# Optimization experiments

Hardware: AMD Instinct MI355X
Metric: run time of the kernel (lower is better)

The kernel has to match this reference:

```python
import jax, jax.numpy as jnp
import numpy as np


def _scan_dir(x, A, B, reverse):
    """First-order linear recurrence h_i = A*h_{i-1} + B*x_i along last axis (W).
    x: [Bsz, C, H, W]; A, B: [C]. reverse=True scans right-to-left but returns
    states in original index order (matching torch scan_backward)."""
    xs = jnp.moveaxis(x, -1, 0)  # [W, Bsz, C, H]
    Ab = A[None, :, None]
    Bb = B[None, :, None]
    def step(h, xi):
        h = Ab * h + Bb * xi
        return h, h
    h0 = jnp.zeros_like(xs[0])
    _, hs = jax.lax.scan(step, h0, xs, reverse=reverse)
    return jnp.moveaxis(hs, 0, -1)  # [Bsz, C, H, W]


def _conv1x1(x, W, b):
    # x: [B,Cin,H,W], W: [Cout,Cin], b: [Cout]
    return jnp.einsum('bchw,dc->bdhw', x, W) + b[None, :, None, None]


def setup_inputs() -> dict:
    key = jax.random.key(0)
    ks = jax.random.split(key, 10)
    B, C, H, W = 8, 64, 128, 128
    D = 128  # hidden_dim
    return {
        'F_in': jax.random.normal(ks[0], (B, C, H, W), dtype=jnp.float32),
        'prior': jax.random.uniform(ks[1], (B, 1, H, W), dtype=jnp.float32),
        'Wi': jax.random.normal(ks[2], (D, C), dtype=jnp.float32) * 0.05,
        'bi': jnp.zeros((D,), dtype=jnp.float32),
        'A_param': jax.random.normal(ks[3], (D,), dtype=jnp.float32),
        'B_param': jax.random.normal(ks[4], (D,), dtype=jnp.float32),
        'alpha': jnp.float32(0.1),
        'gamma': jnp.float32(0.1),
        'Wf': jax.random.normal(ks[5], (D, 4 * D), dtype=jnp.float32) * 0.05,
        'bf': jnp.zeros((D,), dtype=jnp.float32),
        'Wo': jax.random.normal(ks[6], (C, D), dtype=jnp.float32) * 0.05,
        'bo': jnp.zeros((C,), dtype=jnp.float32),
    }


def reference(F_in, prior, Wi, bi, A_param, B_param, alpha, gamma, Wf, bf, Wo, bo):
    # prior has 1 channel, repeated to C channels (prior already matches HxW)
    prior_r = jnp.broadcast_to(prior, F_in.shape)
    F_mod = F_in + alpha * prior_r
    x = _conv1x1(F_mod, Wi, bi)  # [B, D, H, W]
    A = jnp.tanh(A_param)
    Bp = B_param
    h_lr = _scan_dir(x, A, Bp, reverse=False)
    h_rl = _scan_dir(x, A, Bp, reverse=True)
    xt = jnp.swapaxes(x, 2, 3)  # scan over H axis
    h_tb = jnp.swapaxes(_scan_dir(xt, A, Bp, reverse=False), 2, 3)
    h_bt = jnp.swapaxes(_scan_dir(xt, A, Bp, reverse=True), 2, 3)
    h = jnp.concatenate([h_lr, h_rl, h_tb, h_bt], axis=1)  # [B, 4D, H, W]
    h = _conv1x1(h, Wf, bf)   # fusion -> [B, D, H, W]
    out = _conv1x1(h, Wo, bo)  # output_proj -> [B, C, H, W]
    return F_mod + gamma * out
```

## Files before the change

### kernel.cpp

```cpp
#include <hip/hip_runtime.h>
#include <hip/hip_bf16.h>

typedef unsigned int u32;
typedef unsigned short u16;
typedef float f32x2 __attribute__((ext_vector_type(2)));
typedef float f32x4 __attribute__((ext_vector_type(4)));
using bf16x8 = __attribute__((ext_vector_type(8))) short;
using f32x4v = __attribute__((ext_vector_type(4))) float;

#define DEVINL __device__ __forceinline__

constexpr int SCAN_LDS = 32768;
constexpr int XS = 132;
constexpr int LDS_X = 128 * XS * 2;

DEVINL float bf2f(u16 u) { union { u32 i; float f; } v; v.i = ((u32)u) << 16; return v.f; }
DEVINL float bf2f_lo(u32 u) { union { u32 i; float f; } v; v.i = u << 16; return v.f; }
DEVINL float bf2f_hi(u32 u) { union { u32 i; float f; } v; v.i = u & 0xffff0000u; return v.f; }
DEVINL u16 f2bf(float f) {
  __hip_bfloat16 h = __float2bfloat16(f);
  u16 r; __builtin_memcpy(&r, &h, 2); return r;
}
DEVINL u32 pack2(float a, float b) { return (u32)f2bf(a) | ((u32)f2bf(b) << 16); }

__global__ __launch_bounds__(256) void k_pre(
    const float* __restrict__ Wf, const float* __restrict__ Wo,
    const float* __restrict__ bf_, const float* __restrict__ bo,
    const float* __restrict__ A_param, const float* __restrict__ Wi,
    float* __restrict__ A_t, float* __restrict__ beff,
    u16* __restrict__ Mrow, u16* __restrict__ Wi_bf) {
  const int wg = blockIdx.x, t = threadIdx.x;
  if (wg < 128) {
    const int idx = wg * 256 + t;
    const int cout = idx >> 9;
    const int k = idx & 511;
    float s = 0.f;
    for (int d = 0; d < 128; ++d) s = fmaf(Wo[cout * 128 + d], Wf[d * 512 + k], s);
    const int dir = k >> 7, dm = k & 127;
    Mrow[(dir * 64 + cout) * 128 + dm] = f2bf(s);
  } else if (wg == 128) {
    if (t < 128) A_t[t] = tanhf(A_param[t]);
    if (t < 64) {
      float s = bo[t];
      for (int d = 0; d < 128; ++d) s = fmaf(Wo[t * 128 + d], bf_[d], s);
      beff[t] = s;
    }
  } else {
#pragma unroll
    for (int k = 0; k < 32; ++k) {
      const int i = t + k * 256;
      Wi_bf[i] = f2bf(Wi[i]);
    }
  }
}

extern __shared__ char smem[];

template <bool REV>
DEVINL void scan_col128(char* buf, int dp, float A0, float A1, float B0, float B1) {
  float h0 = 0.f, h1 = 0.f;
  const u32 cb = (u32)(dp * 4);
  u32 nx[8];
#pragma unroll
  for (int j = 0; j < 8; ++j) {
    const int i = REV ? (127 - j) : j;
    nx[j] = *(const u32*)(buf + i * 128 + (cb ^ ((u32)((i & 7) << 4))));
  }
  for (int ib = 0; ib < 128; ib += 8) {
    u32 cur[8];
#pragma unroll
    for (int j = 0; j < 8; ++j) cur[j] = nx[j];
    if (ib + 8 < 128) {
#pragma unroll
      for (int j = 0; j < 8; ++j) {
        const int i = REV ? (127 - (ib + 8 + j)) : (ib + 8 + j);
        nx[j] = *(const u32*)(buf + i * 128 + (cb ^ ((u32)((i & 7) << 4))));
      }
    }
#pragma unroll
    for (int j = 0; j < 8; ++j) {
      const int i = REV ? (127 - (ib + j)) : (ib + j);
      h0 = fmaf(A0, h0, B0 * bf2f_lo(cur[j]));
      h1 = fmaf(A1, h1, B1 * bf2f_hi(cur[j]));
      *(u32*)(buf + i * 128 + (cb ^ ((u32)((i & 7) << 4)))) = pack2(h0, h1);
    }
  }
}

DEVINL void combine64(const char* buf, const u16* __restrict__ Mrow, int dir, int e,
                      int lane, int wv, f32x4v (&acc2)[4][2]) {
  const int l15 = lane & 15, kg = lane >> 4;
#pragma unroll
  for (int ks = 0; ks < 2; ++ks) {
    bf16x8 afr[4], bfr[2];
#pragma unroll
    for (int ct = 0; ct < 4; ++ct)
      afr[ct] = *(const bf16x8*)(Mrow + ((size_t)dir * 64 + ct * 16 + l15) * 128 + e * 64 + ks * 32 + kg * 8);
#pragma unroll
    for (int pt = 0; pt < 2; ++pt) {
      const int row = wv * 32 + pt * 16 + l15;
      bfr[pt] = *(const bf16x8*)(buf + row * 128 + ((u32)(ks * 64 + kg * 16) ^ ((u32)((row & 7) << 4))));
    }
#pragma unroll
    for (int ct = 0; ct < 4; ++ct)
#pragma unroll
      for (int pt = 0; pt < 2; ++pt)
        acc2[ct][pt] = __builtin_amdgcn_mfma_f32_16x16x32_bf16(afr[ct], bfr[pt], acc2[ct][pt], 0, 0, 0);
  }
}

DEVINL void acc_to_outs(const f32x4v (&acc2)[4][2], int lane, int wv, char* buf) {
  const int l15 = lane & 15, kg = lane >> 4;
#pragma unroll
  for (int ct = 0; ct < 4; ++ct)
#pragma unroll
    for (int pt = 0; pt < 2; ++pt)
#pragma unroll
      for (int r = 0; r < 4; ++r) {
        const int row = ct * 16 + kg * 4 + r;
        const int col = wv * 32 + pt * 16 + l15;
        *(float*)(buf + row * 512 + ((u32)(col * 4) ^ ((u32)((row & 7) << 4)))) = acc2[ct][pt][r];
      }
}

DEVINL void outs_to_global(const char* buf, u16* __restrict__ og, int t) {
#pragma unroll
  for (int j = 0; j < 16; ++j) {
    const int i = t + j * 256;
    const int c = i >> 6, p2 = (i & 63) * 2;
    const f32x2 v = *(const f32x2*)(buf + c * 512 + ((u32)(p2 * 4) ^ ((u32)((c & 7) << 4))));
    *(u32*)(og + c * 128 + p2) = pack2(v.x, v.y);
  }
}

__global__ __launch_bounds__(256, 5) void k_A(
    const float* __restrict__ F_in, const float* __restrict__ prior,
    const u16* __restrict__ Wi_bf, const float* __restrict__ bi,
    const float* __restrict__ Bp, const float* __restrict__ alpha_p,
    const float* __restrict__ A_t, const u16* __restrict__ Mrow,
    u16* __restrict__ x2, u16* __restrict__ Shp) {
  char* bufA = smem;
  char* bufB = smem + 16384;

  const int t = threadIdx.x;
  const int lane = t & 63, wv = t >> 6, l15 = lane & 15, kg = lane >> 4;
  const int bid = blockIdx.x;
  const int b = bid >> 8, h = (bid >> 1) & 127, e = bid & 1;

  {
    const int w = t & 127, ch = t >> 7;
    const float alpha = alpha_p[0];
    const float pv = prior[(b * 128 + h) * 128 + w];
    const float* Fb = F_in + ((size_t)b * 64 + ch * 32) * 16384 + h * 128 + w;
    const u32 sw = (u32)((w & 7) << 4);
    char* rowp = bufA + w * 128;
#pragma unroll
    for (int q = 0; q < 4; ++q) {
      float fv[8];
#pragma unroll
      for (int j = 0; j < 8; ++j) fv[j] = fmaf(alpha, pv, Fb[(q * 8 + j) * 16384]);
      uint4 pk;
      pk.x = pack2(fv[0], fv[1]); pk.y = pack2(fv[2], fv[3]);
      pk.z = pack2(fv[4], fv[5]); pk.w = pack2(fv[6], fv[7]);
      *(uint4*)(rowp + ((u32)(ch * 64 + q * 16) ^ sw)) = pk;
    }
  }
  __syncthreads();

  bf16x8 aF[2][2];
#pragma unroll
  for (int ks = 0; ks < 2; ++ks)
#pragma unroll
    for (int mt = 0; mt < 2; ++mt) {
      const int row = wv * 32 + mt * 16 + l15;
      aF[ks][mt] = *(const bf16x8*)(bufA + row * 128 + ((u32)(ks * 64 + kg * 16) ^ ((u32)((row & 7) << 4))));
    }
  __syncthreads();

  {
    f32x4v acc[2][4];
#pragma unroll
    for (int mt = 0; mt < 2; ++mt)
#pragma unroll
      for (int nt = 0; nt < 4; ++nt) {
        const float bv = bi[e * 64 + nt * 16 + l15];
        acc[mt][nt] = (f32x4v){ bv, bv, bv, bv };
      }
#pragma unroll
    for (int ks = 0; ks < 2; ++ks)
#pragma unroll
      for (int nt = 0; nt < 4; ++nt) {
        const bf16x8 bWi = *(const bf16x8*)(Wi_bf + (e * 64 + nt * 16 + l15) * 64 + ks * 32 + kg * 8);
        acc[0][nt] = __builtin_amdgcn_mfma_f32_16x16x32_bf16(aF[ks][0], bWi, acc[0][nt], 0, 0, 0);
        acc[1][nt] = __builtin_amdgcn_mfma_f32_16x16x32_bf16(aF[ks][1], bWi, acc[1][nt], 0, 0, 0);
      }
#pragma unroll
    for (int mt = 0; mt < 2; ++mt)
#pragma unroll
      for (int nt = 0; nt < 4; ++nt)
#pragma unroll
        for (int r = 0; r < 4; ++r) {
          const int w = wv * 32 + mt * 16 + kg * 4 + r;
          const u32 col = (u32)((nt * 16 + l15) * 2) ^ ((u32)((w & 7) << 4));
          const u16 v = f2bf(acc[mt][nt][r]);
          *(u16*)(bufA + w * 128 + col) = v;
          *(u16*)(bufB + w * 128 + col) = v;
        }
  }
  __syncthreads();

  {
    u16* xg = x2 + (size_t)bid * 8192;
#pragma unroll
    for (int j = 0; j < 4; ++j) {
      const int idx = t + j * 256;
      const int row = idx >> 3, q = idx & 7;
      const uint4 v = *(const uint4*)(bufB + row * 128 + ((u32)(q * 16) ^ ((u32)((row & 7) << 4))));
      *(uint4*)(xg + row * 64 + q * 8) = v;
    }
  }
  __syncthreads();

  if (wv < 2 && lane < 32) {
    const int dgp = e * 64 + lane * 2;
    const f32x2 a = *(const f32x2*)(A_t + dgp);
    const f32x2 bb = *(const f32x2*)(Bp + dgp);
    if (wv == 0) scan_col128<false>(bufA, lane, a.x, a.y, bb.x, bb.y);
    else         scan_col128<true >(bufB, lane, a.x, a.y, bb.x, bb.y);
  }
  __syncthreads();

  f32x4v acc2[4][2];
#pragma unroll
  for (int i = 0; i < 4; ++i)
#pragma unroll
    for (int j = 0; j < 2; ++j) acc2[i][j] = (f32x4v)0.f;
  combine64(bufA, Mrow, 0, e, lane, wv, acc2);
  combine64(bufB, Mrow, 1, e, lane, wv, acc2);
  __syncthreads();

  acc_to_outs(acc2, lane, wv, smem);
  __syncthreads();

  outs_to_global(smem, Shp + (size_t)bid * 8192, t);
}

__global__ __launch_bounds__(256, 5) void k_B(
    const u16* __restrict__ x2, const float* __restrict__ Bp,
    const float* __restrict__ A_t, const u16* __restrict__ Mrow,
    u16* __restrict__ Svp) {
  char* bufA = smem;
  char* bufB = smem + 16384;
  const int t = threadIdx.x;
  const int lane = t & 63, wv = t >> 6;
  const int bid = blockIdx.x;
  const int b = bid >> 8, w = (bid >> 1) & 127, e = bid & 1;

#pragma unroll
  for (int j = 0; j < 4; ++j) {
    const int idx = t + j * 256;
    const int hh = idx >> 3, q = idx & 7;
    const uint4 v = *(const uint4*)(x2 + ((size_t)((b * 128 + hh) * 2 + e)) * 8192 + w * 64 + q * 8);
    const u32 col = (u32)(q * 16) ^ ((u32)((hh & 7) << 4));
    *(uint4*)(bufA + hh * 128 + col) = v;
    *(uint4*)(bufB + hh * 128 + col) = v;
  }
  __syncthreads();

  if (wv < 2 && lane < 32) {
    const int dgp = e * 64 + lane * 2;
    const f32x2 a = *(const f32x2*)(A_t + dgp);
    const f32x2 bb = *(const f32x2*)(Bp + dgp);
    if (wv == 0) scan_col128<false>(bufA, lane, a.x, a.y, bb.x, bb.y);
    else         scan_col128<true >(bufB, lane, a.x, a.y, bb.x, bb.y);
  }
  __syncthreads();

  f32x4v acc2[4][2];
#pragma unroll
  for (int i = 0; i < 4; ++i)
#pragma unroll
    for (int j = 0; j < 2; ++j) acc2[i][j] = (f32x4v)0.f;
  combine64(bufA, Mrow, 2, e, lane, wv, acc2);
  combine64(bufB, Mrow, 3, e, lane, wv, acc2);
  __syncthreads();

  acc_to_outs(acc2, lane, wv, smem);
  __syncthreads();

  outs_to_global(smem, Svp + (size_t)bid * 8192, t);
}

__global__ __launch_bounds__(256) void k_final(
    const float* __restrict__ F_in, const float* __restrict__ prior,
    const float* __restrict__ alpha_p, const float* __restrict__ gamma_p,
    const float* __restrict__ beff, const u16* __restrict__ Svp,
    const u16* __restrict__ Shp, float* __restrict__ out) {
  u16* Xu = (u16*)smem;
  const int t = threadIdx.x;
  const int bid = blockIdx.x, b = bid >> 6, c = bid & 63;
  const size_t base = (size_t)bid * 16384;

  for (int i = t; i < 2048; i += 256) {
    const int w = i >> 4, q = i & 15;
    const u16* s0 = Svp + ((size_t)((b * 128 + w) * 2)) * 8192 + c * 128 + q * 8;
    const uint4 a4 = *(const uint4*)(s0);
    const uint4 b4 = *(const uint4*)(s0 + 8192);
    const u16* ap = (const u16*)&a4;
    const u16* bp = (const u16*)&b4;
    u32* dst = (u32*)(Xu + w * 132 + q * 8);
#pragma unroll
    for (int k = 0; k < 4; ++k) {
      const float lo = bf2f(ap[k * 2]) + bf2f(bp[k * 2]);
      const float hi = bf2f(ap[k * 2 + 1]) + bf2f(bp[k * 2 + 1]);
      dst[k] = pack2(lo, hi);
    }
  }
  __syncthreads();
  const float alpha = alpha_p[0], gamma = gamma_p[0];
  const float be = beff[c];
  for (int i = t; i < 2048; i += 256) {
    const int hh = i >> 4, w8 = (i & 15) * 8;
    const size_t off = base + hh * 128 + w8;
    const u16* sh0 = Shp + ((size_t)((b * 128 + hh) * 2)) * 8192 + c * 128 + w8;
    const uint4 g0 = *(const uint4*)(sh0);
    const uint4 g1 = *(const uint4*)(sh0 + 8192);
    const u16* p0 = (const u16*)&g0;
    const u16* p1 = (const u16*)&g1;
    const float* Fp = F_in + off;
    float* Op = out + off;
    const float* Pp = prior + (b * 128 + hh) * 128 + w8;
#pragma unroll
    for (int q = 0; q < 8; ++q) {
      const float sv = bf2f(Xu[(w8 + q) * 132 + hh]);
      Op[q] = Fp[q] + alpha * Pp[q] + gamma * (bf2f(p0[q]) + bf2f(p1[q]) + sv + be);
    }
  }
}

extern "C" void kernel_launch(void* const* d_in, const int* in_sizes, int n_in,
                              void* d_out, int out_size, void* d_ws, size_t ws_size,
                              hipStream_t stream) {
  const float* F_in   = (const float*)d_in[0];
  const float* prior  = (const float*)d_in[1];
  const float* Wi     = (const float*)d_in[2];
  const float* bi     = (const float*)d_in[3];
  const float* A_par  = (const float*)d_in[4];
  const float* B_par  = (const float*)d_in[5];
  const float* alpha  = (const float*)d_in[6];
  const float* gamma  = (const float*)d_in[7];
  const float* Wf     = (const float*)d_in[8];
  const float* bf_    = (const float*)d_in[9];
  const float* Wo     = (const float*)d_in[10];
  const float* bo     = (const float*)d_in[11];
  float* out = (float*)d_out;

  char* ws = (char*)d_ws;
  float* A_t   = (float*)ws;
  float* beff  = (float*)(ws + 512);
  u16*   Mrow  = (u16*)(ws + 1024);
  u16*   Wi_bf = (u16*)(ws + 66560);
  u16*   x2    = (u16*)(ws + 82944);
  u16*   Shp   = (u16*)(ws + 82944 + 33554432);
  u16*   Svp   = (u16*)(ws + 82944 + 67108864);

  hipFuncSetAttribute((const void*)k_A, hipFuncAttributeMaxDynamicSharedMemorySize, SCAN_LDS);
  hipFuncSetAttribute((const void*)k_B, hipFuncAttributeMaxDynamicSharedMemorySize, SCAN_LDS);

  k_pre  <<<130, 256, 0, stream>>>(Wf, Wo, bf_, bo, A_par, Wi, A_t, beff, Mrow, Wi_bf);
  k_A    <<<2048, 256, SCAN_LDS, stream>>>(F_in, prior, Wi_bf, bi, B_par, alpha, A_t, Mrow, x2, Shp);
  k_B    <<<2048, 256, SCAN_LDS, stream>>>(x2, B_par, A_t, Mrow, Svp);
  k_final<<<512, 256, LDS_X, stream>>>(F_in, prior, alpha, gamma, beff, Svp, Shp, out);
}
```

Before: 108.7 us.

## Parallelize in-block linear scans across all threads with chunked carry fix-up

Before, each 128-long scan ran serially on 64 of the 256 threads (two half-waves). Now each scan is split into 4 chunks of 32, so all 256 threads do local scans. After a barrier, each chunk computes its carry-in from the earlier chunks' last elements using A^32 and applies p*C corrections. The x tile is also duplicated into bufB during the global copy-out instead of by dual scalar stores. This adds a second LDS pass, an extra barrier and extra bf16 rounding of intermediate chunk states, which changes numerics slightly.

```diff
diff --git a/kernel.cpp b/kernel.cpp
--- a/kernel.cpp
+++ b/kernel.cpp
@@ -57,34 +57,98 @@
 extern __shared__ char smem[];
 
 template <bool REV>
-DEVINL void scan_col128(char* buf, int dp, float A0, float A1, float B0, float B1) {
+DEVINL void scan_local(char* buf, int dp, int chunk, float A0, float A1, float B0, float B1) {
   float h0 = 0.f, h1 = 0.f;
   const u32 cb = (u32)(dp * 4);
+  const int s = chunk * 32;
   u32 nx[8];
 #pragma unroll
   for (int j = 0; j < 8; ++j) {
-    const int i = REV ? (127 - j) : j;
+    const int i = REV ? (127 - (s + j)) : (s + j);
     nx[j] = *(const u32*)(buf + i * 128 + (cb ^ ((u32)((i & 7) << 4))));
   }
-  for (int ib = 0; ib < 128; ib += 8) {
+  for (int ib = 0; ib < 32; ib += 8) {
     u32 cur[8];
 #pragma unroll
     for (int j = 0; j < 8; ++j) cur[j] = nx[j];
-    if (ib + 8 < 128) {
+    if (ib + 8 < 32) {
 #pragma unroll
       for (int j = 0; j < 8; ++j) {
-        const int i = REV ? (127 - (ib + 8 + j)) : (ib + 8 + j);
+        const int i2 = s + ib + 8 + j;
+        const int i = REV ? (127 - i2) : i2;
         nx[j] = *(const u32*)(buf + i * 128 + (cb ^ ((u32)((i & 7) << 4))));
       }
     }
 #pragma unroll
     for (int j = 0; j < 8; ++j) {
-      const int i = REV ? (127 - (ib + j)) : (ib + j);
+      const int i2 = s + ib + j;
+      const int i = REV ? (127 - i2) : i2;
       h0 = fmaf(A0, h0, B0 * bf2f_lo(cur[j]));
       h1 = fmaf(A1, h1, B1 * bf2f_hi(cur[j]));
       *(u32*)(buf + i * 128 + (cb ^ ((u32)((i & 7) << 4)))) = pack2(h0, h1);
     }
   }
+}
+
+template <bool REV>
+DEVINL void scan_fix(char* buf, int dp, int chunk, float A0, float A1) {
+  if (chunk == 0) return;
+  float q0 = A0, q1 = A1;
+#pragma unroll
+  for (int k = 0; k < 5; ++k) { q0 *= q0; q1 *= q1; }
+  const u32 cb = (u32)(dp * 4);
+  float C0 = 0.f, C1 = 0.f;
+  for (int k = 0; k < chunk; ++k) {
+    const int i2 = k * 32 + 31;
+    const int i = REV ? (127 - i2) : i2;
+    const u32 v = *(const u32*)(buf + i * 128 + (cb ^ ((u32)((i & 7) << 4))));
+    C0 = fmaf(C0, q0, bf2f_lo(v));
+    C1 = fmaf(C1, q1, bf2f_hi(v));
+  }
+  float p0 = A0, p1 = A1;
+  const int s = chunk * 32;
+  u32 nx[8];
+#pragma unroll
+  for (int j = 0; j < 8; ++j) {
+    const int i = REV ? (127 - (s + j)) : (s + j);
+    nx[j] = *(const u32*)(buf + i * 128 + (cb ^ ((u32)((i & 7) << 4))));
+  }
+  for (int ib = 0; ib < 32; ib += 8) {
+    u32 cur[8];
+#pragma unroll
+    for (int j = 0; j < 8; ++j) cur[j] = nx[j];
+    if (ib + 8 < 32) {
+#pragma unroll
+      for (int j = 0; j < 8; ++j) {
+        const int i2 = s + ib + 8 + j;
+        const int i = REV ? (127 - i2) : i2;
+        nx[j] = *(const u32*)(buf + i * 128 + (cb ^ ((u32)((i & 7) << 4))));
+      }
+    }
+#pragma unroll
+    for (int j = 0; j < 8; ++j) {
+      const int i2 = s + ib + j;
+      const int i = REV ? (127 - i2) : i2;
+      const float h0 = fmaf(p0, C0, bf2f_lo(cur[j]));
+      const float h1 = fmaf(p1, C1, bf2f_hi(cur[j]));
+      *(u32*)(buf + i * 128 + (cb ^ ((u32)((i & 7) << 4)))) = pack2(h0, h1);
+      p0 *= A0; p1 *= A1;
+    }
+  }
+}
+
+DEVINL void run_scans(char* bufA, char* bufB, int t, int e,
+                      const float* __restrict__ A_t, const float* __restrict__ Bp) {
+  const int dp = t & 31, chunk = (t >> 5) & 3, dir = t >> 7;
+  const int dgp = e * 64 + dp * 2;
+  const f32x2 a = *(const f32x2*)(A_t + dgp);
+  const f32x2 bb = *(const f32x2*)(Bp + dgp);
+  char* sb = dir ? bufB : bufA;
+  if (dir == 0) scan_local<false>(sb, dp, chunk, a.x, a.y, bb.x, bb.y);
+  else          scan_local<true >(sb, dp, chunk, a.x, a.y, bb.x, bb.y);
+  __syncthreads();
+  if (dir == 0) scan_fix<false>(sb, dp, chunk, a.x, a.y);
+  else          scan_fix<true >(sb, dp, chunk, a.x, a.y);
 }
 
 DEVINL void combine64(const char* buf, const u16* __restrict__ Mrow, int dir, int e,
@@ -202,9 +266,7 @@
         for (int r = 0; r < 4; ++r) {
           const int w = wv * 32 + mt * 16 + kg * 4 + r;
           const u32 col = (u32)((nt * 16 + l15) * 2) ^ ((u32)((w & 7) << 4));
-          const u16 v = f2bf(acc[mt][nt][r]);
-          *(u16*)(bufA + w * 128 + col) = v;
-          *(u16*)(bufB + w * 128 + col) = v;
+          *(u16*)(bufA + w * 128 + col) = f2bf(acc[mt][nt][r]);
         }
   }
   __syncthreads();
@@ -215,19 +277,15 @@
     for (int j = 0; j < 4; ++j) {
       const int idx = t + j * 256;
       const int row = idx >> 3, q = idx & 7;
-      const uint4 v = *(const uint4*)(bufB + row * 128 + ((u32)(q * 16) ^ ((u32)((row & 7) << 4))));
+      const u32 off = (u32)(q * 16) ^ ((u32)((row & 7) << 4));
+      const uint4 v = *(const uint4*)(bufA + row * 128 + off);
       *(uint4*)(xg + row * 64 + q * 8) = v;
-    }
-  }
-  __syncthreads();
-
-  if (wv < 2 && lane < 32) {
-    const int dgp = e * 64 + lane * 2;
-    const f32x2 a = *(const f32x2*)(A_t + dgp);
-    const f32x2 bb = *(const f32x2*)(Bp + dgp);
-    if (wv == 0) scan_col128<false>(bufA, lane, a.x, a.y, bb.x, bb.y);
-    else         scan_col128<true >(bufB, lane, a.x, a.y, bb.x, bb.y);
-  }
+      *(uint4*)(bufB + row * 128 + off) = v;
+    }
+  }
+  __syncthreads();
+
+  run_scans(bufA, bufB, t, e, A_t, Bp);
   __syncthreads();
 
   f32x4v acc2[4][2];
@@ -267,13 +325,7 @@
   }
   __syncthreads();
 
-  if (wv < 2 && lane < 32) {
-    const int dgp = e * 64 + lane * 2;
-    const f32x2 a = *(const f32x2*)(A_t + dgp);
-    const f32x2 bb = *(const f32x2*)(Bp + dgp);
-    if (wv == 0) scan_col128<false>(bufA, lane, a.x, a.y, bb.x, bb.y);
-    else         scan_col128<true >(bufB, lane, a.x, a.y, bb.x, bb.y);
-  }
+  run_scans(bufA, bufB, t, e, A_t, Bp);
   __syncthreads();
 
   f32x4v acc2[4][2];
```

After: 98.61 us. 1.1x faster.
